# Performance work log

Measured on AMD Instinct MI355X. Metric: run time of the kernel, lower is better.

The kernel has to match this reference:

```python
import jax, jax.numpy as jnp
import numpy as np

NUM_LAYER = 6
NUM_HEADS = 1
NEG_INF = -1e9


def setup_inputs() -> dict:
    key = jax.random.key(0)
    ks = jax.random.split(key, 8)
    bs, C, N = 8, 128, 2048
    H0 = (jax.random.uniform(ks[0], (bs, N, N)) < 0.2).astype(jnp.float32)
    vertex_feat = jax.random.normal(ks[1], (bs, C, N), dtype=jnp.float32)
    edge_feat = jax.random.normal(ks[2], (bs, C, N), dtype=jnp.float32)
    s = 1.0 / np.sqrt(C)  # Conv1d(k=1) default init scale
    Wq = jax.random.uniform(ks[3], (C, C), minval=-s, maxval=s, dtype=jnp.float32)
    bq = jax.random.uniform(ks[4], (C,), minval=-s, maxval=s, dtype=jnp.float32)
    Wk = jax.random.uniform(ks[5], (C, C), minval=-s, maxval=s, dtype=jnp.float32)
    bk = jax.random.uniform(ks[6], (C,), minval=-s, maxval=s, dtype=jnp.float32)
    return {"H0": H0, "vertex_feat": vertex_feat, "edge_feat": edge_feat,
            "Wq": Wq, "bq": bq, "Wk": Wk, "bk": bk, "it": 4}


def reference(H0, vertex_feat, edge_feat, Wq, bq, Wk, bk, it):
    bs, N, _ = H0.shape
    C = Wq.shape[0]
    head = NUM_HEADS
    dh = C // head
    # Conv1d kernel_size=1 == pointwise linear over channel dim
    Q = (jnp.einsum('oc,bcn->bon', Wq, vertex_feat) + bq[None, :, None]).reshape(bs, head, dh, N)
    K = (jnp.einsum('oc,bcn->bon', Wk, edge_feat) + bk[None, :, None]).reshape(bs, head, dh, N)
    att = jnp.einsum('bhco,bhci->bhoi', Q, K) / np.sqrt(dh)  # [bs,h,N,N]
    mask = jnp.where(H0 > 0, 0.0, NEG_INF)                   # masked_fill(1-H0)
    score = jax.nn.sigmoid(att + mask[:, None]).sum(axis=1) / head  # [bs,N,N]
    # mask_score, choice='topk': keep top-k scores per row
    k = round(N * 0.1 * (NUM_LAYER - 1 - it))
    topk_vals = jax.lax.top_k(score, k)[0]          # [bs,N,k]
    a_min = topk_vals[..., -1:]                     # k-th largest per row
    W = jnp.where(score >= a_min, score, 0.0)
    H = jnp.where(W > 0, H0, 0.0)
    # degree-normalization matrices (diag_embed of 1/deg, inf -> 0)
    deg_E = H.sum(axis=1)   # [bs,N] edge degrees
    deg_V = H.sum(axis=2)   # [bs,N] vertex degrees
    De_n_1 = jax.vmap(jnp.diag)(jnp.where(deg_E != 0, 1.0 / deg_E, 0.0))
    Dv_n_1 = jax.vmap(jnp.diag)(jnp.where(deg_V != 0, 1.0 / deg_V, 0.0))
    # edge weights: L2-normalized column sums of W (F.normalize, eps=1e-12)
    W_edge = W.sum(axis=1)
    nrm = jnp.maximum(jnp.linalg.norm(W_edge, axis=1, keepdims=True), 1e-12)
    W_edge = (W_edge / nrm)[:, :, None]  # [bs,N,1]
    return H, W, De_n_1, Dv_n_1, W_edge
```

## Files before the change

### kernel.cpp

```cpp
#include <hip/hip_runtime.h>
#include <math.h>

#define NUM_LAYER 6

typedef __attribute__((ext_vector_type(8))) short short8;
typedef __attribute__((ext_vector_type(4))) float f32x4;
typedef unsigned short u16;

__device__ __forceinline__ void split3(float x, u16& h, u16& m, u16& l) {
  unsigned ux = __float_as_uint(x);
  h = (u16)(ux >> 16);
  float r1 = x - __uint_as_float(ux & 0xFFFF0000u);
  unsigned u1 = __float_as_uint(r1);
  m = (u16)(u1 >> 16);
  float r2 = r1 - __uint_as_float(u1 & 0xFFFF0000u);
  l = (u16)(__float_as_uint(r2) >> 16);
}

__global__ __launch_bounds__(256) void qk_gemm_split(
    const float* __restrict__ Wq, const float* __restrict__ bq,
    const float* __restrict__ vf,
    const float* __restrict__ Wk, const float* __restrict__ bk,
    const float* __restrict__ ef,
    u16* __restrict__ Qh, u16* __restrict__ Qm, u16* __restrict__ Ql,
    u16* __restrict__ Kh, u16* __restrict__ Km, u16* __restrict__ Kl,
    int C, int N, int bs) {
  int which = (int)blockIdx.y >= bs;
  int b = (int)blockIdx.y - (which ? bs : 0);
  const float* Wm = which ? Wk : Wq;
  const float* bias = which ? bk : bq;
  const float* X = (which ? ef : vf) + (size_t)b * C * N;
  u16* Ph = which ? Kh : Qh;
  u16* Pm = which ? Km : Qm;
  u16* Pl = which ? Kl : Ql;
  int n0 = blockIdx.x * 128;
  __shared__ float As[8][128];
  __shared__ float Xs[8][128];
  int t = threadIdx.x;
  int tx = t & 15, ty = t >> 4;
  int ao = t >> 1, ac = (t & 1) * 4;
  int lk = t >> 5, lj = (t & 31) * 4;
  float acc[8][8] = {};
  for (int c0 = 0; c0 < C; c0 += 8) {
    __syncthreads();
    float4 wv = *(const float4*)&Wm[(size_t)ao * C + c0 + ac];
    As[ac + 0][ao] = wv.x; As[ac + 1][ao] = wv.y;
    As[ac + 2][ao] = wv.z; As[ac + 3][ao] = wv.w;
    *(float4*)&Xs[lk][lj] = *(const float4*)&X[(size_t)(c0 + lk) * N + n0 + lj];
    __syncthreads();
#pragma unroll
    for (int kk = 0; kk < 8; ++kk) {
      float a[8], bb[8];
      *(float4*)&a[0]  = *(const float4*)&As[kk][ty * 4];
      *(float4*)&a[4]  = *(const float4*)&As[kk][64 + ty * 4];
      *(float4*)&bb[0] = *(const float4*)&Xs[kk][tx * 4];
      *(float4*)&bb[4] = *(const float4*)&Xs[kk][64 + tx * 4];
#pragma unroll
      for (int i = 0; i < 8; ++i)
#pragma unroll
        for (int j = 0; j < 8; ++j)
          acc[i][j] = fmaf(a[i], bb[j], acc[i][j]);
    }
  }
  float bv[8];
#pragma unroll
  for (int i = 0; i < 8; ++i) bv[i] = bias[(i >> 2) * 64 + ty * 4 + (i & 3)];
#pragma unroll
  for (int j = 0; j < 8; ++j) {
    int n = n0 + tx * 4 + (j & 3) + (j >> 2) * 64;
    size_t nb = ((size_t)b * N + n) * C;
#pragma unroll
    for (int g = 0; g < 2; ++g) {
      int r0 = g * 64 + ty * 4;
      ushort4 hv, mv, lv;
      split3(acc[g * 4 + 0][j] + bv[g * 4 + 0], hv.x, mv.x, lv.x);
      split3(acc[g * 4 + 1][j] + bv[g * 4 + 1], hv.y, mv.y, lv.y);
      split3(acc[g * 4 + 2][j] + bv[g * 4 + 2], hv.z, mv.z, lv.z);
      split3(acc[g * 4 + 3][j] + bv[g * 4 + 3], hv.w, mv.w, lv.w);
      *(ushort4*)&Ph[nb + r0] = hv;
      *(ushort4*)&Pm[nb + r0] = mv;
      *(ushort4*)&Pl[nb + r0] = lv;
    }
  }
}

__global__ __launch_bounds__(256) void att_mfma(
    const u16* __restrict__ Qh, const u16* __restrict__ Qm,
    const u16* __restrict__ Ql, const u16* __restrict__ Kh,
    const u16* __restrict__ Km, const u16* __restrict__ Kl,
    const float* __restrict__ H0, float* __restrict__ score,
    int C, int N, float rsdh) {
  int b = blockIdx.z;
  int o0 = blockIdx.y * 128, i0 = blockIdx.x * 128;
  __shared__ u16 sm[6][128][40];
  __shared__ float et[4][16][68];
  int t = threadIdx.x;
  int wave = t >> 6, lane = t & 63, quad = lane >> 4, lr = lane & 15;
  int wo = wave >> 1, wi = wave & 1;
  f32x4 acc[4][4];
#pragma unroll
  for (int mi = 0; mi < 4; ++mi)
#pragma unroll
    for (int ni = 0; ni < 4; ++ni) acc[mi][ni] = (f32x4){0.f, 0.f, 0.f, 0.f};

  int ro = t >> 1, ch = (t & 1) * 16;
  size_t qbase = ((size_t)b * N + o0 + ro) * C + ch;
  size_t kbase = ((size_t)b * N + i0 + ro) * C + ch;
  const u16* gq[3] = {Qh, Qm, Ql};
  const u16* gk[3] = {Kh, Km, Kl};

  for (int c0 = 0; c0 < C; c0 += 32) {
    __syncthreads();
#pragma unroll
    for (int a = 0; a < 3; ++a) {
      const uint4* src = (const uint4*)(gq[a] + qbase + c0);
      *(uint4*)&sm[a][ro][ch] = src[0];
      *(uint4*)&sm[a][ro][ch + 8] = src[1];
      const uint4* srk = (const uint4*)(gk[a] + kbase + c0);
      *(uint4*)&sm[3 + a][ro][ch] = srk[0];
      *(uint4*)&sm[3 + a][ro][ch + 8] = srk[1];
    }
    __syncthreads();
    short8 bh[4], bm[4], bl[4];
#pragma unroll
    for (int ni = 0; ni < 4; ++ni) {
      int row = wi * 64 + ni * 16 + lr;
      bh[ni] = *(const short8*)&sm[3][row][quad * 8];
      bm[ni] = *(const short8*)&sm[4][row][quad * 8];
      bl[ni] = *(const short8*)&sm[5][row][quad * 8];
    }
#pragma unroll
    for (int mi = 0; mi < 4; ++mi) {
      int row = wo * 64 + mi * 16 + lr;
      short8 ah = *(const short8*)&sm[0][row][quad * 8];
      short8 am = *(const short8*)&sm[1][row][quad * 8];
      short8 al = *(const short8*)&sm[2][row][quad * 8];
#pragma unroll
      for (int ni = 0; ni < 4; ++ni) {
        f32x4 c = acc[mi][ni];
        c = __builtin_amdgcn_mfma_f32_16x16x32_bf16(ah, bl[ni], c, 0, 0, 0);
        c = __builtin_amdgcn_mfma_f32_16x16x32_bf16(al, bh[ni], c, 0, 0, 0);
        c = __builtin_amdgcn_mfma_f32_16x16x32_bf16(am, bm[ni], c, 0, 0, 0);
        c = __builtin_amdgcn_mfma_f32_16x16x32_bf16(ah, bm[ni], c, 0, 0, 0);
        c = __builtin_amdgcn_mfma_f32_16x16x32_bf16(am, bh[ni], c, 0, 0, 0);
        c = __builtin_amdgcn_mfma_f32_16x16x32_bf16(ah, bh[ni], c, 0, 0, 0);
        acc[mi][ni] = c;
      }
    }
  }
  const float* Hb = H0 + (size_t)b * N * N;
  float* Sb = score + (size_t)b * N * N;
  int rr = lane >> 2, seg = lane & 3;
#pragma unroll
  for (int mi = 0; mi < 4; ++mi) {
#pragma unroll
    for (int ni = 0; ni < 4; ++ni)
#pragma unroll
      for (int r = 0; r < 4; ++r)
        et[wave][quad * 4 + r][ni * 16 + lr] = acc[mi][ni][r];
    __syncthreads();
    int o = o0 + wo * 64 + mi * 16 + rr;
    const float* hr = Hb + (size_t)o * N + i0 + wi * 64;
    float* sr = Sb + (size_t)o * N + i0 + wi * 64;
#pragma unroll
    for (int j = 0; j < 4; ++j) {
      int col = j * 16 + seg * 4;
      float4 c = *(const float4*)&et[wave][rr][col];
      float4 h = *(const float4*)&hr[col];
      float4 oV;
      oV.x = (h.x > 0.f) ? 1.f / (1.f + __expf(-c.x * rsdh)) : 0.f;
      oV.y = (h.y > 0.f) ? 1.f / (1.f + __expf(-c.y * rsdh)) : 0.f;
      oV.z = (h.z > 0.f) ? 1.f / (1.f + __expf(-c.z * rsdh)) : 0.f;
      oV.w = (h.w > 0.f) ? 1.f / (1.f + __expf(-c.w * rsdh)) : 0.f;
      *(float4*)&sr[col] = oV;
    }
    __syncthreads();
  }
}

template <int V4>
__global__ __launch_bounds__(512) void topk_select(
    float* __restrict__ scoreW, float* __restrict__ Hout,
    float* __restrict__ degV, float* __restrict__ PE, float* __restrict__ PW,
    const int* __restrict__ itp, int N) {
  int b = blockIdx.y;
  int strip = blockIdx.x;
  int t = threadIdx.x;
  int wave = t >> 6, lane = t & 63;
  int row = strip * 8 + wave;
  size_t rowoff = ((size_t)b * N + row) * N;
  extern __shared__ float cols[];
  float* colE = cols;
  float* colW = cols + N;
  for (int i = t; i < 2 * N; i += 512) cols[i] = 0.f;

  float4 v4[V4];
#pragma unroll
  for (int q = 0; q < V4; ++q)
    v4[q] = *(const float4*)(scoreW + rowoff + 4 * lane + (q << 8));
  int itv = *itp;
  int k = (int)floor((double)N * 0.1 * (double)(NUM_LAYER - 1 - itv) + 0.5);
  unsigned lo = 0u, hi = 0x3F800000u;
  while (lo < hi) {
    unsigned mid = lo + ((hi - lo + 1u) >> 1);
    float thr = __uint_as_float(mid);
    int c = 0;
#pragma unroll
    for (int q = 0; q < V4; ++q) {
      c += (v4[q].x >= thr) ? 1 : 0;
      c += (v4[q].y >= thr) ? 1 : 0;
      c += (v4[q].z >= thr) ? 1 : 0;
      c += (v4[q].w >= thr) ? 1 : 0;
    }
#pragma unroll
    for (int off = 1; off < 64; off <<= 1) c += __shfl_xor(c, off);
    if (c >= k) lo = mid; else hi = mid - 1u;
  }
  float am = __uint_as_float(lo);
  __syncthreads();

  float rs = 0.f;
#pragma unroll
  for (int q = 0; q < V4; ++q) {
    int c0 = 4 * lane + (q << 8);
    float4 s = v4[q];
    float4 w, h;
    w.x = (s.x >= am) ? s.x : 0.f; h.x = (w.x > 0.f) ? 1.f : 0.f;
    w.y = (s.y >= am) ? s.y : 0.f; h.y = (w.y > 0.f) ? 1.f : 0.f;
    w.z = (s.z >= am) ? s.z : 0.f; h.z = (w.z > 0.f) ? 1.f : 0.f;
    w.w = (s.w >= am) ? s.w : 0.f; h.w = (w.w > 0.f) ? 1.f : 0.f;
    *(float4*)(scoreW + rowoff + c0) = w;
    *(float4*)(Hout + rowoff + c0) = h;
    rs += h.x + h.y + h.z + h.w;
    if (h.x != 0.f) { atomicAdd(&colE[c0 + 0], 1.f); atomicAdd(&colW[c0 + 0], w.x); }
    if (h.y != 0.f) { atomicAdd(&colE[c0 + 1], 1.f); atomicAdd(&colW[c0 + 1], w.y); }
    if (h.z != 0.f) { atomicAdd(&colE[c0 + 2], 1.f); atomicAdd(&colW[c0 + 2], w.z); }
    if (h.w != 0.f) { atomicAdd(&colE[c0 + 3], 1.f); atomicAdd(&colW[c0 + 3], w.w); }
  }
#pragma unroll
  for (int off = 32; off; off >>= 1) rs += __shfl_down(rs, off);
  if (lane == 0) degV[b * N + row] = rs;
  __syncthreads();
  int S = N >> 3;
  size_t pbase = ((size_t)b * S + strip) * N;
  for (int c = 4 * t; c < N; c += 2048) {
    *(float4*)(PE + pbase + c) = *(const float4*)&colE[c];
    *(float4*)(PW + pbase + c) = *(const float4*)&colW[c];
  }
}

__global__ __launch_bounds__(256) void col_reduce(
    const float* __restrict__ PE, const float* __restrict__ PW,
    float* __restrict__ degE, float* __restrict__ We, int N, int S) {
  int b = blockIdx.y;
  int col = blockIdx.x * 256 + threadIdx.x;
  float se0 = 0.f, se1 = 0.f, sw0 = 0.f, sw1 = 0.f;
  for (int s = 0; s < S; s += 4) {
    size_t o0 = ((size_t)b * S + s) * N + col;
    se0 += PE[o0];           sw0 += PW[o0];
    se1 += PE[o0 + N];       sw1 += PW[o0 + N];
    se0 += PE[o0 + 2 * (size_t)N]; sw0 += PW[o0 + 2 * (size_t)N];
    se1 += PE[o0 + 3 * (size_t)N]; sw1 += PW[o0 + 3 * (size_t)N];
  }
  degE[b * N + col] = se0 + se1;
  We[b * N + col] = sw0 + sw1;
}

__global__ __launch_bounds__(256) void dedv_fill(
    float* __restrict__ De, float* __restrict__ Dv,
    const float* __restrict__ degE, const float* __restrict__ degV, int N) {
  int arr = blockIdx.z;
  int b = blockIdx.y;
  int r0 = blockIdx.x * 8;
  float* out = (arr ? Dv : De) + (size_t)b * N * N;
  const float* deg = (arr ? degV : degE) + b * N;
  int t = threadIdx.x;
#pragma unroll
  for (int r = r0; r < r0 + 8; ++r) {
    float d = deg[r];
    float inv = (d != 0.f) ? 1.f / d : 0.f;
    size_t rowoff = (size_t)r * N;
    for (int c4 = t * 4; c4 < N; c4 += 1024) {
      float4 v = {0.f, 0.f, 0.f, 0.f};
      unsigned dd = (unsigned)(r - c4);
      if (dd < 4u) ((float*)&v)[dd] = inv;
      *(float4*)&out[rowoff + c4] = v;
    }
  }
}

__global__ __launch_bounds__(256) void wedge_norm(
    const float* __restrict__ We, float* __restrict__ out, int N) {
  int b = blockIdx.x;
  int t = threadIdx.x;
  const float* w = We + (size_t)b * N;
  float ss = 0.f;
  for (int i = t; i < N; i += 256) { float x = w[i]; ss += x * x; }
  for (int off = 32; off; off >>= 1) ss += __shfl_down(ss, off);
  __shared__ float p[4];
  if ((t & 63) == 0) p[t >> 6] = ss;
  __syncthreads();
  float tot = p[0] + p[1] + p[2] + p[3];
  float nrm = fmaxf(sqrtf(tot), 1e-12f);
  for (int i = t; i < N; i += 256) out[(size_t)b * N + i] = w[i] / nrm;
}

extern "C" void kernel_launch(void* const* d_in, const int* in_sizes, int n_in,
                              void* d_out, int out_size, void* d_ws, size_t ws_size,
                              hipStream_t stream) {
  const float* H0 = (const float*)d_in[0];
  const float* vf = (const float*)d_in[1];
  const float* ef = (const float*)d_in[2];
  const float* Wq = (const float*)d_in[3];
  const float* bq = (const float*)d_in[4];
  const float* Wk = (const float*)d_in[5];
  const float* bk = (const float*)d_in[6];
  const int* itp  = (const int*)d_in[7];

  int C = (int)(sqrt((double)in_sizes[3]) + 0.5);
  long long ratio = (long long)in_sizes[0] / in_sizes[1];
  int N = (int)(C * ratio);
  int bs = (int)(in_sizes[1] / ((long long)C * N));
  size_t bNN = (size_t)bs * N * N;
  size_t bNC = (size_t)bs * N * C;
  int S = N >> 3;
  size_t pElems = (size_t)bs * S * N;

  float* outH  = (float*)d_out;
  float* outW  = outH + bNN;
  float* outDe = outW + bNN;
  float* outDv = outDe + bNN;
  float* outWe = outDv + bNN;

  size_t bsN = (size_t)bs * N;
  float* degE = (float*)d_ws;
  float* degV = degE + bsN;
  float* We   = degV + bsN;
  u16* splits;
  float* PE;
  float* PW;
  size_t need = 3 * bsN * sizeof(float) + 6 * bNC * sizeof(u16) +
                2 * pElems * sizeof(float);
  if (ws_size >= need) {
    splits = (u16*)(We + bsN);
    PE = (float*)(splits + 6 * bNC);
    PW = PE + pElems;
  } else {
    splits = (u16*)outDe;
    PE = outDv;
    PW = PE + pElems;
  }
  u16* Qh = splits;
  u16* Qm = Qh + bNC;
  u16* Ql = Qm + bNC;
  u16* Kh = Ql + bNC;
  u16* Km = Kh + bNC;
  u16* Kl = Km + bNC;

  float rsdh = (float)(1.0 / sqrt((double)C));
  size_t colsBytes = 2 * (size_t)N * sizeof(float);

  qk_gemm_split<<<dim3(N / 128, 2 * bs), 256, 0, stream>>>(
      Wq, bq, vf, Wk, bk, ef, Qh, Qm, Ql, Kh, Km, Kl, C, N, bs);
  att_mfma<<<dim3(N / 128, N / 128, bs), 256, 0, stream>>>(
      Qh, Qm, Ql, Kh, Km, Kl, H0, outW, C, N, rsdh);
  if (N == 2048)
    topk_select<8><<<dim3(S, bs), 512, colsBytes, stream>>>(
        outW, outH, degV, PE, PW, itp, N);
  else if (N == 1024)
    topk_select<4><<<dim3(S, bs), 512, colsBytes, stream>>>(
        outW, outH, degV, PE, PW, itp, N);
  else
    topk_select<16><<<dim3(S, bs), 512, colsBytes, stream>>>(
        outW, outH, degV, PE, PW, itp, N);
  col_reduce<<<dim3(N / 256, bs), 256, 0, stream>>>(PE, PW, degE, We, N, S);
  dedv_fill<<<dim3(N / 8, bs, 2), 256, 0, stream>>>(outDe, outDv, degE,
                                                    degV, N);
  wedge_norm<<<dim3(bs), 256, 0, stream>>>(We, outWe, N);
}
```

Measured before the change: 868.3 us.

## Replace per-strip LDS atomic column partials with direct column-sum pass over W

```diff
diff --git a/kernel.cpp b/kernel.cpp
--- a/kernel.cpp
+++ b/kernel.cpp
@@ -92,8 +92,11 @@
     int C, int N, float rsdh) {
   int b = blockIdx.z;
   int o0 = blockIdx.y * 128, i0 = blockIdx.x * 128;
-  __shared__ u16 sm[6][128][40];
-  __shared__ float et[4][16][68];
+  union ShU {
+    u16 sm[6][128][34];
+    float et[4][16][68];
+  };
+  __shared__ ShU sh;
   int t = threadIdx.x;
   int wave = t >> 6, lane = t & 63, quad = lane >> 4, lr = lane & 15;
   int wo = wave >> 1, wi = wave & 1;
@@ -114,27 +117,27 @@
 #pragma unroll
     for (int a = 0; a < 3; ++a) {
       const uint4* src = (const uint4*)(gq[a] + qbase + c0);
-      *(uint4*)&sm[a][ro][ch] = src[0];
-      *(uint4*)&sm[a][ro][ch + 8] = src[1];
+      *(uint4*)&sh.sm[a][ro][ch] = src[0];
+      *(uint4*)&sh.sm[a][ro][ch + 8] = src[1];
       const uint4* srk = (const uint4*)(gk[a] + kbase + c0);
-      *(uint4*)&sm[3 + a][ro][ch] = srk[0];
-      *(uint4*)&sm[3 + a][ro][ch + 8] = srk[1];
+      *(uint4*)&sh.sm[3 + a][ro][ch] = srk[0];
+      *(uint4*)&sh.sm[3 + a][ro][ch + 8] = srk[1];
     }
     __syncthreads();
     short8 bh[4], bm[4], bl[4];
 #pragma unroll
     for (int ni = 0; ni < 4; ++ni) {
       int row = wi * 64 + ni * 16 + lr;
-      bh[ni] = *(const short8*)&sm[3][row][quad * 8];
-      bm[ni] = *(const short8*)&sm[4][row][quad * 8];
-      bl[ni] = *(const short8*)&sm[5][row][quad * 8];
+      bh[ni] = *(const short8*)&sh.sm[3][row][quad * 8];
+      bm[ni] = *(const short8*)&sh.sm[4][row][quad * 8];
+      bl[ni] = *(const short8*)&sh.sm[5][row][quad * 8];
     }
 #pragma unroll
     for (int mi = 0; mi < 4; ++mi) {
       int row = wo * 64 + mi * 16 + lr;
-      short8 ah = *(const short8*)&sm[0][row][quad * 8];
-      short8 am = *(const short8*)&sm[1][row][quad * 8];
-      short8 al = *(const short8*)&sm[2][row][quad * 8];
+      short8 ah = *(const short8*)&sh.sm[0][row][quad * 8];
+      short8 am = *(const short8*)&sh.sm[1][row][quad * 8];
+      short8 al = *(const short8*)&sh.sm[2][row][quad * 8];
 #pragma unroll
       for (int ni = 0; ni < 4; ++ni) {
         f32x4 c = acc[mi][ni];
@@ -148,6 +151,7 @@
       }
     }
   }
+  __syncthreads();
   const float* Hb = H0 + (size_t)b * N * N;
   float* Sb = score + (size_t)b * N * N;
   int rr = lane >> 2, seg = lane & 3;
@@ -157,15 +161,14 @@
     for (int ni = 0; ni < 4; ++ni)
 #pragma unroll
       for (int r = 0; r < 4; ++r)
-        et[wave][quad * 4 + r][ni * 16 + lr] = acc[mi][ni][r];
-    __syncthreads();
+        sh.et[wave][quad * 4 + r][ni * 16 + lr] = acc[mi][ni][r];
     int o = o0 + wo * 64 + mi * 16 + rr;
     const float* hr = Hb + (size_t)o * N + i0 + wi * 64;
     float* sr = Sb + (size_t)o * N + i0 + wi * 64;
 #pragma unroll
     for (int j = 0; j < 4; ++j) {
       int col = j * 16 + seg * 4;
-      float4 c = *(const float4*)&et[wave][rr][col];
+      float4 c = *(const float4*)&sh.et[wave][rr][col];
       float4 h = *(const float4*)&hr[col];
       float4 oV;
       oV.x = (h.x > 0.f) ? 1.f / (1.f + __expf(-c.x * rsdh)) : 0.f;
@@ -174,25 +177,19 @@
       oV.w = (h.w > 0.f) ? 1.f / (1.f + __expf(-c.w * rsdh)) : 0.f;
       *(float4*)&sr[col] = oV;
     }
-    __syncthreads();
   }
 }
 
 template <int V4>
 __global__ __launch_bounds__(512) void topk_select(
     float* __restrict__ scoreW, float* __restrict__ Hout,
-    float* __restrict__ degV, float* __restrict__ PE, float* __restrict__ PW,
-    const int* __restrict__ itp, int N) {
+    float* __restrict__ degV, const int* __restrict__ itp, int N) {
   int b = blockIdx.y;
   int strip = blockIdx.x;
   int t = threadIdx.x;
   int wave = t >> 6, lane = t & 63;
   int row = strip * 8 + wave;
   size_t rowoff = ((size_t)b * N + row) * N;
-  extern __shared__ float cols[];
-  float* colE = cols;
-  float* colW = cols + N;
-  for (int i = t; i < 2 * N; i += 512) cols[i] = 0.f;
 
   float4 v4[V4];
 #pragma unroll
@@ -217,7 +214,6 @@
     if (c >= k) lo = mid; else hi = mid - 1u;
   }
   float am = __uint_as_float(lo);
-  __syncthreads();
 
   float rs = 0.f;
 #pragma unroll
@@ -232,38 +228,30 @@
     *(float4*)(scoreW + rowoff + c0) = w;
     *(float4*)(Hout + rowoff + c0) = h;
     rs += h.x + h.y + h.z + h.w;
-    if (h.x != 0.f) { atomicAdd(&colE[c0 + 0], 1.f); atomicAdd(&colW[c0 + 0], w.x); }
-    if (h.y != 0.f) { atomicAdd(&colE[c0 + 1], 1.f); atomicAdd(&colW[c0 + 1], w.y); }
-    if (h.z != 0.f) { atomicAdd(&colE[c0 + 2], 1.f); atomicAdd(&colW[c0 + 2], w.z); }
-    if (h.w != 0.f) { atomicAdd(&colE[c0 + 3], 1.f); atomicAdd(&colW[c0 + 3], w.w); }
   }
 #pragma unroll
   for (int off = 32; off; off >>= 1) rs += __shfl_down(rs, off);
   if (lane == 0) degV[b * N + row] = rs;
-  __syncthreads();
-  int S = N >> 3;
-  size_t pbase = ((size_t)b * S + strip) * N;
-  for (int c = 4 * t; c < N; c += 2048) {
-    *(float4*)(PE + pbase + c) = *(const float4*)&colE[c];
-    *(float4*)(PW + pbase + c) = *(const float4*)&colW[c];
-  }
-}
-
-__global__ __launch_bounds__(256) void col_reduce(
-    const float* __restrict__ PE, const float* __restrict__ PW,
-    float* __restrict__ degE, float* __restrict__ We, int N, int S) {
+}
+
+__global__ __launch_bounds__(256) void col_sum(
+    const float* __restrict__ W, float* __restrict__ degE,
+    float* __restrict__ We, int N) {
   int b = blockIdx.y;
   int col = blockIdx.x * 256 + threadIdx.x;
-  float se0 = 0.f, se1 = 0.f, sw0 = 0.f, sw1 = 0.f;
-  for (int s = 0; s < S; s += 4) {
-    size_t o0 = ((size_t)b * S + s) * N + col;
-    se0 += PE[o0];           sw0 += PW[o0];
-    se1 += PE[o0 + N];       sw1 += PW[o0 + N];
-    se0 += PE[o0 + 2 * (size_t)N]; sw0 += PW[o0 + 2 * (size_t)N];
-    se1 += PE[o0 + 3 * (size_t)N]; sw1 += PW[o0 + 3 * (size_t)N];
-  }
-  degE[b * N + col] = se0 + se1;
-  We[b * N + col] = sw0 + sw1;
+  const float* Wb = W + (size_t)b * N * N + col;
+  float c0 = 0.f, c1 = 0.f, s0 = 0.f, s1 = 0.f;
+  for (int r = 0; r < N; r += 4) {
+    float w0 = Wb[(size_t)r * N];
+    float w1 = Wb[(size_t)(r + 1) * N];
+    float w2 = Wb[(size_t)(r + 2) * N];
+    float w3 = Wb[(size_t)(r + 3) * N];
+    s0 += w0 + w1; s1 += w2 + w3;
+    c0 += (w0 > 0.f ? 1.f : 0.f) + (w1 > 0.f ? 1.f : 0.f);
+    c1 += (w2 > 0.f ? 1.f : 0.f) + (w3 > 0.f ? 1.f : 0.f);
+  }
+  degE[b * N + col] = c0 + c1;
+  We[b * N + col] = s0 + s1;
 }
 
 __global__ __launch_bounds__(256) void dedv_fill(
@@ -324,7 +312,6 @@
   size_t bNN = (size_t)bs * N * N;
   size_t bNC = (size_t)bs * N * C;
   int S = N >> 3;
-  size_t pElems = (size_t)bs * S * N;
 
   float* outH  = (float*)d_out;
   float* outW  = outH + bNN;
@@ -337,18 +324,11 @@
   float* degV = degE + bsN;
   float* We   = degV + bsN;
   u16* splits;
-  float* PE;
-  float* PW;
-  size_t need = 3 * bsN * sizeof(float) + 6 * bNC * sizeof(u16) +
-                2 * pElems * sizeof(float);
+  size_t need = 3 * bsN * sizeof(float) + 6 * bNC * sizeof(u16);
   if (ws_size >= need) {
     splits = (u16*)(We + bsN);
-    PE = (float*)(splits + 6 * bNC);
-    PW = PE + pElems;
   } else {
     splits = (u16*)outDe;
-    PE = outDv;
-    PW = PE + pElems;
   }
   u16* Qh = splits;
   u16* Qm = Qh + bNC;
@@ -358,22 +338,18 @@
   u16* Kl = Km + bNC;
 
   float rsdh = (float)(1.0 / sqrt((double)C));
-  size_t colsBytes = 2 * (size_t)N * sizeof(float);
 
   qk_gemm_split<<<dim3(N / 128, 2 * bs), 256, 0, stream>>>(
       Wq, bq, vf, Wk, bk, ef, Qh, Qm, Ql, Kh, Km, Kl, C, N, bs);
   att_mfma<<<dim3(N / 128, N / 128, bs), 256, 0, stream>>>(
       Qh, Qm, Ql, Kh, Km, Kl, H0, outW, C, N, rsdh);
   if (N == 2048)
-    topk_select<8><<<dim3(S, bs), 512, colsBytes, stream>>>(
-        outW, outH, degV, PE, PW, itp, N);
+    topk_select<8><<<dim3(S, bs), 512, 0, stream>>>(outW, outH, degV, itp, N);
   else if (N == 1024)
-    topk_select<4><<<dim3(S, bs), 512, colsBytes, stream>>>(
-        outW, outH, degV, PE, PW, itp, N);
+    topk_select<4><<<dim3(S, bs), 512, 0, stream>>>(outW, outH, degV, itp, N);
   else
-    topk_select<16><<<dim3(S, bs), 512, colsBytes, stream>>>(
-        outW, outH, degV, PE, PW, itp, N);
-  col_reduce<<<dim3(N / 256, bs), 256, 0, stream>>>(PE, PW, degE, We, N, S);
+    topk_select<16><<<dim3(S, bs), 512, 0, stream>>>(outW, outH, degV, itp, N);
+  col_sum<<<dim3(N / 256, bs), 256, 0, stream>>>(outW, degE, We, N);
   dedv_fill<<<dim3(N / 8, bs, 2), 256, 0, stream>>>(outDe, outDv, degE,
                                                     degV, N);
   wedge_norm<<<dim3(bs), 256, 0, stream>>>(We, outWe, N);
```

After: 986.3 us. 1.14x slower.
